# Kernel optimization log

Hardware: AMD Instinct MI355X
Metric: run time of the kernel (lower is better)

Reference implementation:

```python
import jax, jax.numpy as jnp
import numpy as np

N, FEAT, NCLS = 8192, 1024, 64


def setup_inputs() -> dict:
    key = jax.random.key(0)
    k1, k2, k3, k4, k5, k6 = jax.random.split(key, 6)
    x = jax.random.normal(k1, (N, FEAT), dtype=jnp.float32)
    adj = jax.random.uniform(k2, (N, N), dtype=jnp.float32)  # pairwise distances
    stdv1 = 1.0 / np.sqrt(FEAT)
    W1 = jax.random.uniform(k3, (FEAT, FEAT), jnp.float32, -stdv1, stdv1)
    b1 = jax.random.uniform(k4, (FEAT,), jnp.float32, -stdv1, stdv1)
    W2 = jax.random.uniform(k5, (FEAT, NCLS), jnp.float32, -stdv1, stdv1)
    b2 = jax.random.uniform(k6, (NCLS,), jnp.float32, -stdv1, stdv1)
    alpha = jnp.full((1,), 0.3, dtype=jnp.float32)
    return {"x": x, "adj": adj, "W1": W1, "b1": b1, "W2": W2, "b2": b2,
            "alpha": alpha, "K": 32}


def reference(x, adj, W1, b1, W2, b2, alpha, K):
    # --- top-K smallest-distance neighbor selection per row ---
    neg_vals, idx = jax.lax.top_k(-adj, K)        # K smallest adj entries per row
    vals = -neg_vals                              # [N, K] distances
    w = jnp.exp(-alpha[0] * vals)                 # 1 / exp(alpha * d)
    w = w / jnp.sum(w, axis=1, keepdims=True)     # row-normalize edge weights

    def spmm(h):
        # sparse A @ h using top-K edge list: out[i] = sum_k w[i,k] * h[idx[i,k]]
        return jnp.einsum('nk,nkf->nf', w, h[idx])

    # 2-layer GCN path of SimTSC (eval mode: dropout is identity)
    h = jax.nn.relu(spmm(x @ W1) + b1)            # [N, FEAT]
    out = spmm(h @ W2) + b2                       # [N, NCLS]
    return jax.nn.log_softmax(out, axis=1)
```

## Files before the change

### kernel.cpp

```cpp
#include <hip/hip_runtime.h>

typedef __bf16 bf16_t;
typedef __bf16 bf16x4 __attribute__((ext_vector_type(4)));
typedef __bf16 bf16x8 __attribute__((ext_vector_type(8)));
typedef float  f32x4  __attribute__((ext_vector_type(4)));

typedef const __attribute__((address_space(1))) void gvoid_t;
typedef __attribute__((address_space(3))) void lvoid_t;

#define N_NODES 8192
#define FEAT    1024
#define NCLS    64
#define TK      32

__device__ __forceinline__ float wave_min_f32(float v) {
  int x = __float_as_int(v), t;
#define STEPF(ctrl) t = __builtin_amdgcn_update_dpp(x, x, ctrl, 0xf, 0xf, false); \
                    v = fminf(v, __int_as_float(t)); x = __float_as_int(v);
  STEPF(0x111)
  STEPF(0x112)
  STEPF(0x114)
  STEPF(0x118)
  STEPF(0x142)
  STEPF(0x143)
#undef STEPF
  return __int_as_float(__builtin_amdgcn_readlane(x, 63));
}

__device__ __forceinline__ unsigned wave_min_u32(unsigned v) {
  int x = (int)v, t;
#define STEPU(ctrl) t = __builtin_amdgcn_update_dpp(x, x, ctrl, 0xf, 0xf, false); \
                    x = (int)((unsigned)x < (unsigned)t ? (unsigned)x : (unsigned)t);
  STEPU(0x111)
  STEPU(0x112)
  STEPU(0x114)
  STEPU(0x118)
  STEPU(0x142)
  STEPU(0x143)
#undef STEPU
  return (unsigned)__builtin_amdgcn_readlane(x, 63);
}

__global__ __launch_bounds__(256) void topk_kernel(const float* __restrict__ adj,
                                                   const float* __restrict__ alphap,
                                                   const float* __restrict__ x,
                                                   bf16_t* __restrict__ x_bf,
                                                   int* __restrict__ idx_out,
                                                   float* __restrict__ w_out,
                                                   const float* __restrict__ W1,
                                                   bf16_t* __restrict__ W1t,
                                                   const float* __restrict__ W2,
                                                   bf16_t* __restrict__ W2t) {
  const int tid = threadIdx.x;
  __shared__ float tile[64][65];
  __shared__ float svals[256];
  __shared__ int   sidx[256];
  __shared__ int   scnt;

  if (blockIdx.x >= N_NODES) {
    const int tb = blockIdx.x - N_NODES;
    const int bxi = tb % 17, by = tb / 17;
    const float* in;
    bf16_t* out;
    int cols, bx;
    if (bxi < 16) { in = W1; out = W1t; cols = FEAT; bx = bxi; }
    else          { in = W2; out = W2t; cols = NCLS; bx = 0; }
#pragma unroll
    for (int i = 0; i < 16; ++i) {
      int li = i * 256 + tid;
      int r = li >> 6, c = li & 63;
      tile[r][c] = in[(size_t)(by * 64 + r) * cols + bx * 64 + c];
    }
    __syncthreads();
#pragma unroll
    for (int i = 0; i < 16; ++i) {
      int li = i * 256 + tid;
      int r = li >> 6, c = li & 63;
      out[(size_t)(bx * 64 + r) * FEAT + by * 64 + c] = (__bf16)tile[c][r];
    }
    return;
  }

  const int row = blockIdx.x;
  {
    const float4 v = ((const float4*)(x + (size_t)row * FEAT))[tid];
    bf16x4 o;
    o[0] = (__bf16)v.x; o[1] = (__bf16)v.y; o[2] = (__bf16)v.z; o[3] = (__bf16)v.w;
    ((bf16x4*)(x_bf + (size_t)row * FEAT))[tid] = o;
  }

  const float* arow = adj + (size_t)row * N_NODES;
  float thr = 1.0f / 128.0f;
  int cnt = 0;
  for (int attempt = 0; attempt < 24; ++attempt) {
    __syncthreads();
    if (tid == 0) scnt = 0;
    __syncthreads();
#pragma unroll
    for (int v = 0; v < 8; ++v) {
      int vi = v * 256 + tid;
      float4 q = ((const float4*)arow)[vi];
      int base = vi * 4;
      if (q.x < thr) { int p = atomicAdd(&scnt, 1); if (p < 256) { svals[p] = q.x; sidx[p] = base;     } }
      if (q.y < thr) { int p = atomicAdd(&scnt, 1); if (p < 256) { svals[p] = q.y; sidx[p] = base + 1; } }
      if (q.z < thr) { int p = atomicAdd(&scnt, 1); if (p < 256) { svals[p] = q.z; sidx[p] = base + 2; } }
      if (q.w < thr) { int p = atomicAdd(&scnt, 1); if (p < 256) { svals[p] = q.w; sidx[p] = base + 3; } }
    }
    __syncthreads();
    cnt = scnt;
    if (cnt >= TK && cnt <= 256) break;
    thr = (cnt < TK) ? thr * 2.0f : thr * 0.5f;
  }
  const int M = cnt < 256 ? cnt : 256;

  if (tid < 64) {
    const int lane = tid;
    const float INF = __int_as_float(0x7f800000);
    float cv[4];
    int   ci[4];
#pragma unroll
    for (int j = 0; j < 4; ++j) {
      int slot = lane + j * 64;
      if (slot < M) { cv[j] = svals[slot]; ci[j] = sidx[slot]; }
      else          { cv[j] = INF;         ci[j] = 0x7fffffff; }
    }
    float selv = 0.f;
    int   seli = 0;
    for (int k = 0; k < TK; ++k) {
      const float lv = fminf(fminf(cv[0], cv[1]), fminf(cv[2], cv[3]));
      const float wv = wave_min_f32(lv);
      unsigned li = 0xffffffffu;
#pragma unroll
      for (int j = 0; j < 4; ++j)
        if (cv[j] == wv) li = li < (unsigned)ci[j] ? li : (unsigned)ci[j];
      const unsigned wi = wave_min_u32(li);
      if (lane == k) { selv = wv; seli = (int)wi; }
#pragma unroll
      for (int j = 0; j < 4; ++j)
        if (cv[j] == wv && (unsigned)ci[j] == wi) cv[j] = INF;
    }
    const float a = alphap[0];
    const float e = (lane < TK) ? expf(-a * selv) : 0.0f;
    float ssum = e;
#pragma unroll
    for (int off = 1; off < 64; off <<= 1) ssum += __shfl_xor(ssum, off);
    if (lane < TK) {
      idx_out[(size_t)row * TK + lane] = seli & (N_NODES - 1);
      w_out[(size_t)row * TK + lane]   = e / ssum;
    }
  }
}

__global__ __launch_bounds__(256, 2) void gemm1_kernel(const bf16_t* __restrict__ A,
                                                       const bf16_t* __restrict__ Bt,
                                                       bf16_t* __restrict__ C) {
  constexpr int BM = 128, BN = 128, Kd = FEAT;
  constexpr int LDSA = BM * 64;
  constexpr int LDSB = BN * 64;
  __shared__ char lds[2][LDSA + LDSB];
  const int tid = threadIdx.x;
  const int wid = tid >> 6, lane = tid & 63;
  const int b = blockIdx.x;
  const int xcd = b & 7, j = b >> 3;
  const int bm0 = (xcd * 8 + (j >> 3)) * BM;
  const int bn0 = (j & 7) * BN;
  const int wr = wid >> 1, wc = wid & 1;
  constexpr int WM = BM / 2, WN = BN / 2;
  constexpr int NMI = WM / 16, NNI = WN / 16;

  auto stage = [&](int buf, int t) {
    const int k0 = t * 32;
#pragma unroll
    for (int li = 0; li < BM / 64; ++li) {
      const int rb = wid * (BM / 4) + li * 16;
      const int r = rb + (lane >> 2);
      const int sdat = (lane & 3) ^ (r & 3);
      const bf16_t* g = A + (size_t)(bm0 + r) * Kd + k0 + sdat * 8;
      __builtin_amdgcn_global_load_lds((gvoid_t*)g, (lvoid_t*)&lds[buf][rb * 64], 16, 0, 0);
    }
#pragma unroll
    for (int li = 0; li < BN / 64; ++li) {
      const int rb = wid * (BN / 4) + li * 16;
      const int r = rb + (lane >> 2);
      const int sdat = (lane & 3) ^ (r & 3);
      const bf16_t* g = Bt + (size_t)(bn0 + r) * Kd + k0 + sdat * 8;
      __builtin_amdgcn_global_load_lds((gvoid_t*)g, (lvoid_t*)&lds[buf][LDSA + rb * 64], 16, 0, 0);
    }
  };

  f32x4 acc[NMI][NNI];
#pragma unroll
  for (int mi = 0; mi < NMI; ++mi)
#pragma unroll
    for (int ni = 0; ni < NNI; ++ni) acc[mi][ni] = (f32x4){0.f, 0.f, 0.f, 0.f};

  const int nT = Kd / 32;
  stage(0, 0);
  __syncthreads();
  for (int t = 0; t < nT; ++t) {
    const int cur = t & 1;
    if (t + 1 < nT) stage(cur ^ 1, t + 1);
    const char* la = &lds[cur][0];
    const char* lb = &lds[cur][LDSA];
    const int s = lane >> 4;
    bf16x8 af[NMI], bfr[NNI];
#pragma unroll
    for (int mi = 0; mi < NMI; ++mi) {
      const int m = wr * WM + mi * 16 + (lane & 15);
      af[mi] = *(const bf16x8*)(la + m * 64 + ((s ^ (m & 3)) * 16));
    }
#pragma unroll
    for (int ni = 0; ni < NNI; ++ni) {
      const int n = wc * WN + ni * 16 + (lane & 15);
      bfr[ni] = *(const bf16x8*)(lb + n * 64 + ((s ^ (n & 3)) * 16));
    }
#pragma unroll
    for (int mi = 0; mi < NMI; ++mi)
#pragma unroll
      for (int ni = 0; ni < NNI; ++ni)
        acc[mi][ni] = __builtin_amdgcn_mfma_f32_16x16x32_bf16(af[mi], bfr[ni], acc[mi][ni], 0, 0, 0);
    __syncthreads();
  }

#pragma unroll
  for (int mi = 0; mi < NMI; ++mi)
#pragma unroll
    for (int ni = 0; ni < NNI; ++ni)
#pragma unroll
      for (int j4 = 0; j4 < 4; ++j4) {
        const int r = bm0 + wr * WM + mi * 16 + (lane >> 4) * 4 + j4;
        const int c = bn0 + wc * WN + ni * 16 + (lane & 15);
        C[(size_t)r * FEAT + c] = (__bf16)acc[mi][ni][j4];
      }
}

#define SROWS  16
#define SCHUNK 128
#define NCHUNK 8
__global__ __launch_bounds__(256) void spmm_gemm2_kernel(const bf16_t* __restrict__ xW1,
                                                         const int* __restrict__ idxm,
                                                         const float* __restrict__ wm,
                                                         const float* __restrict__ b1,
                                                         const bf16_t* __restrict__ W2t,
                                                         bf16_t* __restrict__ part) {
  const int tid = threadIdx.x;
  const int c  = blockIdx.x & (NCHUNK - 1);
  const int rg = blockIdx.x >> 3;
  const int r0 = rg * SROWS;
  const int f0 = c * SCHUNK;
  __shared__ int    snb[SROWS][TK];
  __shared__ float  swt[SROWS][TK];
  __shared__ bf16_t hls[SROWS][SCHUNK];
  ((int2*)&snb[0][0])[tid]   = ((const int2*)(idxm + (size_t)r0 * TK))[tid];
  ((float2*)&swt[0][0])[tid] = ((const float2*)(wm + (size_t)r0 * TK))[tid];
  __syncthreads();
  const int wid = tid >> 6, lane = tid & 63;
  const int gr = tid >> 4;
  const int gc = (tid & 15) * 8;

  float a[8];
#pragma unroll
  for (int j = 0; j < 8; ++j) a[j] = 0.f;
#pragma unroll 8
  for (int k = 0; k < TK; ++k) {
    const bf16x8 v = *(const bf16x8*)(xW1 + (size_t)snb[gr][k] * FEAT + f0 + gc);
    const float wk = swt[gr][k];
#pragma unroll
    for (int j = 0; j < 8; ++j) a[j] += wk * (float)v[j];
  }
  const float4 b0 = ((const float4*)(b1 + f0 + gc))[0];
  const float4 b1v = ((const float4*)(b1 + f0 + gc))[1];
  bf16x8 o0;
  o0[0] = (__bf16)fmaxf(a[0] + b0.x, 0.f);
  o0[1] = (__bf16)fmaxf(a[1] + b0.y, 0.f);
  o0[2] = (__bf16)fmaxf(a[2] + b0.z, 0.f);
  o0[3] = (__bf16)fmaxf(a[3] + b0.w, 0.f);
  o0[4] = (__bf16)fmaxf(a[4] + b1v.x, 0.f);
  o0[5] = (__bf16)fmaxf(a[5] + b1v.y, 0.f);
  o0[6] = (__bf16)fmaxf(a[6] + b1v.z, 0.f);
  o0[7] = (__bf16)fmaxf(a[7] + b1v.w, 0.f);
  const int g0 = (gc >> 3);
  char* hb = (char*)&hls[0][0];
  *(bf16x8*)(hb + gr * (SCHUNK * 2) + ((g0 ^ (gr & 7)) * 16)) = o0;

  const int s = lane >> 4;
  const int m = lane & 15;
  const int n = wid * 16 + (lane & 15);
  bf16x8 bfr[SCHUNK / 32];
#pragma unroll
  for (int ks = 0; ks < SCHUNK / 32; ++ks)
    bfr[ks] = *(const bf16x8*)(W2t + (size_t)n * FEAT + f0 + ks * 32 + s * 8);
  __syncthreads();

  f32x4 acc = (f32x4){0.f, 0.f, 0.f, 0.f};
  const char* hr = (char*)&hls[0][0] + m * (SCHUNK * 2);
#pragma unroll
  for (int ks = 0; ks < SCHUNK / 32; ++ks) {
    const int g = ks * 4 + s;
    const bf16x8 afrag = *(const bf16x8*)(hr + ((g ^ (m & 7)) * 16));
    acc = __builtin_amdgcn_mfma_f32_16x16x32_bf16(afrag, bfr[ks], acc, 0, 0, 0);
  }
#pragma unroll
  for (int j = 0; j < 4; ++j) {
    const int r = r0 + (lane >> 4) * 4 + j;
    const int col = wid * 16 + (lane & 15);
    part[((size_t)c * N_NODES + r) * NCLS + col] = (__bf16)acc[j];
  }
}

__global__ __launch_bounds__(256) void reduce8_kernel(const bf16_t* __restrict__ part,
                                                      float* __restrict__ out2) {
  const int i = blockIdx.x * 256 + threadIdx.x;
  float s[8];
  {
    const bf16x8 p = ((const bf16x8*)part)[i];
#pragma unroll
    for (int j = 0; j < 8; ++j) s[j] = (float)p[j];
  }
#pragma unroll
  for (int c = 1; c < NCHUNK; ++c) {
    const bf16x8 p = ((const bf16x8*)(part + (size_t)c * N_NODES * NCLS))[i];
#pragma unroll
    for (int j = 0; j < 8; ++j) s[j] += (float)p[j];
  }
  float4 lo, hi;
  lo.x = s[0]; lo.y = s[1]; lo.z = s[2]; lo.w = s[3];
  hi.x = s[4]; hi.y = s[5]; hi.z = s[6]; hi.w = s[7];
  ((float4*)out2)[i * 2]     = lo;
  ((float4*)out2)[i * 2 + 1] = hi;
}

__global__ __launch_bounds__(256) void final_kernel(const float* __restrict__ out2,
                                                    const int* __restrict__ idxm,
                                                    const float* __restrict__ wm,
                                                    const float* __restrict__ b2,
                                                    float* __restrict__ out) {
  const int wid = threadIdx.x >> 6, lane = threadIdx.x & 63;
  const int row = blockIdx.x * 4 + wid;
  const int kk = lane & 31;
  const float wv = wm[(size_t)row * TK + kk];
  const int   iv = idxm[(size_t)row * TK + kk];
  float acc = 0.f;
#pragma unroll 8
  for (int k = 0; k < TK; ++k) {
    const float wk = __shfl(wv, k);
    const int   ik = __shfl(iv, k);
    acc += wk * out2[(size_t)ik * NCLS + lane];
  }
  const float logit = acc + b2[lane];
  float m = logit;
#pragma unroll
  for (int off = 1; off < 64; off <<= 1) m = fmaxf(m, __shfl_xor(m, off));
  const float e = expf(logit - m);
  float ssum = e;
#pragma unroll
  for (int off = 1; off < 64; off <<= 1) ssum += __shfl_xor(ssum, off);
  out[(size_t)row * NCLS + lane] = (logit - m) - logf(ssum);
}

extern "C" void kernel_launch(void* const* d_in, const int* in_sizes, int n_in,
                              void* d_out, int out_size, void* d_ws, size_t ws_size,
                              hipStream_t stream) {
  (void)in_sizes; (void)n_in; (void)out_size; (void)ws_size;
  const float* x     = (const float*)d_in[0];
  const float* adj   = (const float*)d_in[1];
  const float* W1    = (const float*)d_in[2];
  const float* b1    = (const float*)d_in[3];
  const float* W2    = (const float*)d_in[4];
  const float* b2    = (const float*)d_in[5];
  const float* alpha = (const float*)d_in[6];

  char* ws = (char*)d_ws;
  const size_t MB = 1024 * 1024;
  bf16_t* x_bf = (bf16_t*)(ws + 0 * MB);
  bf16_t* xW1  = (bf16_t*)(ws + 16 * MB);
  bf16_t* W1t  = (bf16_t*)(ws + 48 * MB);
  bf16_t* W2t  = (bf16_t*)(ws + 50 * MB);
  float*  out2 = (float*)(ws + 51 * MB);
  int*    idxm = (int*)(ws + 53 * MB);
  float*  wm   = (float*)(ws + 54 * MB);
  bf16_t* part = (bf16_t*)(ws + 56 * MB);

  topk_kernel<<<dim3(N_NODES + 272), dim3(256), 0, stream>>>(
      adj, alpha, x, x_bf, idxm, wm, W1, W1t, W2, W2t);
  gemm1_kernel<<<dim3(512), dim3(256), 0, stream>>>(x_bf, W1t, xW1);
  spmm_gemm2_kernel<<<dim3((N_NODES / SROWS) * NCHUNK), dim3(256), 0, stream>>>(
      xW1, idxm, wm, b1, W2t, part);
  reduce8_kernel<<<dim3(N_NODES * NCLS / 8 / 256), dim3(256), 0, stream>>>(part, out2);
  final_kernel<<<dim3(N_NODES / 4), dim3(256), 0, stream>>>(out2, idxm, wm, b2, (float*)d_out);
}
```

Before: 135.0 us.

## Fuse top-K selection with the first GEMM into one interleaved kernel

The x conversion and weight transposes move into a small prep kernel. Top-K row selection and the x@W1 GEMM tiles are merged into one launch, with one GEMM block interleaved among every 16 top-K blocks. The bandwidth-bound adjacency scan can then overlap with MFMA-bound GEMM work, and one launch boundary goes away. In exchange, top-K blocks now reserve the GEMM's large LDS allocation and run at the GEMM's occupancy bound, which may cut how many scan blocks fit per CU.

```diff
diff --git a/kernel.cpp b/kernel.cpp
--- a/kernel.cpp
+++ b/kernel.cpp
@@ -41,73 +41,164 @@
   return (unsigned)__builtin_amdgcn_readlane(x, 63);
 }
 
-__global__ __launch_bounds__(256) void topk_kernel(const float* __restrict__ adj,
-                                                   const float* __restrict__ alphap,
-                                                   const float* __restrict__ x,
-                                                   bf16_t* __restrict__ x_bf,
-                                                   int* __restrict__ idx_out,
-                                                   float* __restrict__ w_out,
-                                                   const float* __restrict__ W1,
+__global__ __launch_bounds__(256) void prep_kernel(const float* __restrict__ W1,
                                                    bf16_t* __restrict__ W1t,
                                                    const float* __restrict__ W2,
-                                                   bf16_t* __restrict__ W2t) {
+                                                   bf16_t* __restrict__ W2t,
+                                                   const float* __restrict__ x,
+                                                   bf16_t* __restrict__ x_bf) {
   const int tid = threadIdx.x;
+  const int b = blockIdx.x;
+  if (b < 2048) {
+#pragma unroll
+    for (int i = 0; i < 4; ++i) {
+      const int idx = b * 1024 + i * 256 + tid;
+      const float4 v = ((const float4*)x)[idx];
+      bf16x4 o;
+      o[0] = (__bf16)v.x; o[1] = (__bf16)v.y; o[2] = (__bf16)v.z; o[3] = (__bf16)v.w;
+      ((bf16x4*)x_bf)[idx] = o;
+    }
+    return;
+  }
   __shared__ float tile[64][65];
-  __shared__ float svals[256];
-  __shared__ int   sidx[256];
-  __shared__ int   scnt;
-
-  if (blockIdx.x >= N_NODES) {
-    const int tb = blockIdx.x - N_NODES;
-    const int bxi = tb % 17, by = tb / 17;
-    const float* in;
-    bf16_t* out;
-    int cols, bx;
-    if (bxi < 16) { in = W1; out = W1t; cols = FEAT; bx = bxi; }
-    else          { in = W2; out = W2t; cols = NCLS; bx = 0; }
-#pragma unroll
-    for (int i = 0; i < 16; ++i) {
-      int li = i * 256 + tid;
-      int r = li >> 6, c = li & 63;
-      tile[r][c] = in[(size_t)(by * 64 + r) * cols + bx * 64 + c];
-    }
+  const int tb = b - 2048;
+  const int bxi = tb % 17, by = tb / 17;
+  const float* in;
+  bf16_t* out;
+  int cols, bx;
+  if (bxi < 16) { in = W1; out = W1t; cols = FEAT; bx = bxi; }
+  else          { in = W2; out = W2t; cols = NCLS; bx = 0; }
+#pragma unroll
+  for (int i = 0; i < 16; ++i) {
+    int li = i * 256 + tid;
+    int r = li >> 6, c = li & 63;
+    tile[r][c] = in[(size_t)(by * 64 + r) * cols + bx * 64 + c];
+  }
+  __syncthreads();
+#pragma unroll
+  for (int i = 0; i < 16; ++i) {
+    int li = i * 256 + tid;
+    int r = li >> 6, c = li & 63;
+    out[(size_t)(bx * 64 + r) * FEAT + by * 64 + c] = (__bf16)tile[c][r];
+  }
+}
+
+#define FUSED_BLOCKS (512 * 17)
+__global__ __launch_bounds__(256, 2) void fused_kernel(const float* __restrict__ adj,
+                                                       const float* __restrict__ alphap,
+                                                       const bf16_t* __restrict__ x_bf,
+                                                       const bf16_t* __restrict__ W1t,
+                                                       bf16_t* __restrict__ xW1,
+                                                       int* __restrict__ idx_out,
+                                                       float* __restrict__ w_out) {
+  constexpr int BM = 128, BN = 128, Kd = FEAT;
+  constexpr int LDSA = BM * 64;
+  constexpr int LDSB = BN * 64;
+  __shared__ char smem[2 * (LDSA + LDSB)];
+  const int tid = threadIdx.x;
+  const int b = blockIdx.x;
+  const int j = b / 17;
+
+  if (b % 17 == 0) {
+    auto lds = (char(*)[LDSA + LDSB])smem;
+    const int wid = tid >> 6, lane = tid & 63;
+    const int xcd = j & 7, jj = j >> 3;
+    const int bm0 = (xcd * 8 + (jj >> 3)) * BM;
+    const int bn0 = (jj & 7) * BN;
+    const int wr = wid >> 1, wc = wid & 1;
+    constexpr int WM = BM / 2, WN = BN / 2;
+    constexpr int NMI = WM / 16, NNI = WN / 16;
+
+    auto stage = [&](int buf, int t) {
+      const int k0 = t * 32;
+#pragma unroll
+      for (int li = 0; li < BM / 64; ++li) {
+        const int rb = wid * (BM / 4) + li * 16;
+        const int r = rb + (lane >> 2);
+        const int sdat = (lane & 3) ^ (r & 3);
+        const bf16_t* g = x_bf + (size_t)(bm0 + r) * Kd + k0 + sdat * 8;
+        __builtin_amdgcn_global_load_lds((gvoid_t*)g, (lvoid_t*)&lds[buf][rb * 64], 16, 0, 0);
+      }
+#pragma unroll
+      for (int li = 0; li < BN / 64; ++li) {
+        const int rb = wid * (BN / 4) + li * 16;
+        const int r = rb + (lane >> 2);
+        const int sdat = (lane & 3) ^ (r & 3);
+        const bf16_t* g = W1t + (size_t)(bn0 + r) * Kd + k0 + sdat * 8;
+        __builtin_amdgcn_global_load_lds((gvoid_t*)g, (lvoid_t*)&lds[buf][LDSA + rb * 64], 16, 0, 0);
+      }
+    };
+
+    f32x4 acc[NMI][NNI];
+#pragma unroll
+    for (int mi = 0; mi < NMI; ++mi)
+#pragma unroll
+      for (int ni = 0; ni < NNI; ++ni) acc[mi][ni] = (f32x4){0.f, 0.f, 0.f, 0.f};
+
+    const int nT = Kd / 32;
+    stage(0, 0);
     __syncthreads();
-#pragma unroll
-    for (int i = 0; i < 16; ++i) {
-      int li = i * 256 + tid;
-      int r = li >> 6, c = li & 63;
-      out[(size_t)(bx * 64 + r) * FEAT + by * 64 + c] = (__bf16)tile[c][r];
-    }
+    for (int t = 0; t < nT; ++t) {
+      const int cur = t & 1;
+      if (t + 1 < nT) stage(cur ^ 1, t + 1);
+      const char* la = &lds[cur][0];
+      const char* lb = &lds[cur][LDSA];
+      const int s = lane >> 4;
+      bf16x8 af[NMI], bfr[NNI];
+#pragma unroll
+      for (int mi = 0; mi < NMI; ++mi) {
+        const int m = wr * WM + mi * 16 + (lane & 15);
+        af[mi] = *(const bf16x8*)(la + m * 64 + ((s ^ (m & 3)) * 16));
+      }
+#pragma unroll
+      for (int ni = 0; ni < NNI; ++ni) {
+        const int n = wc * WN + ni * 16 + (lane & 15);
+        bfr[ni] = *(const bf16x8*)(lb + n * 64 + ((s ^ (n & 3)) * 16));
+      }
+#pragma unroll
+      for (int mi = 0; mi < NMI; ++mi)
+#pragma unroll
+        for (int ni = 0; ni < NNI; ++ni)
+          acc[mi][ni] = __builtin_amdgcn_mfma_f32_16x16x32_bf16(af[mi], bfr[ni], acc[mi][ni], 0, 0, 0);
+      __syncthreads();
+    }
+
+#pragma unroll
+    for (int mi = 0; mi < NMI; ++mi)
+#pragma unroll
+      for (int ni = 0; ni < NNI; ++ni)
+#pragma unroll
+        for (int j4 = 0; j4 < 4; ++j4) {
+          const int r = bm0 + wr * WM + mi * 16 + (lane >> 4) * 4 + j4;
+          const int c = bn0 + wc * WN + ni * 16 + (lane & 15);
+          xW1[(size_t)r * FEAT + c] = (__bf16)acc[mi][ni][j4];
+        }
     return;
   }
 
-  const int row = blockIdx.x;
-  {
-    const float4 v = ((const float4*)(x + (size_t)row * FEAT))[tid];
-    bf16x4 o;
-    o[0] = (__bf16)v.x; o[1] = (__bf16)v.y; o[2] = (__bf16)v.z; o[3] = (__bf16)v.w;
-    ((bf16x4*)(x_bf + (size_t)row * FEAT))[tid] = o;
-  }
-
+  float* svals = (float*)smem;
+  int*   sidx  = (int*)(smem + 1024);
+  int*   scnt  = (int*)(smem + 2048);
+  const int row = b - j - 1;
   const float* arow = adj + (size_t)row * N_NODES;
   float thr = 1.0f / 128.0f;
   int cnt = 0;
   for (int attempt = 0; attempt < 24; ++attempt) {
     __syncthreads();
-    if (tid == 0) scnt = 0;
+    if (tid == 0) *scnt = 0;
     __syncthreads();
 #pragma unroll
     for (int v = 0; v < 8; ++v) {
       int vi = v * 256 + tid;
       float4 q = ((const float4*)arow)[vi];
       int base = vi * 4;
-      if (q.x < thr) { int p = atomicAdd(&scnt, 1); if (p < 256) { svals[p] = q.x; sidx[p] = base;     } }
-      if (q.y < thr) { int p = atomicAdd(&scnt, 1); if (p < 256) { svals[p] = q.y; sidx[p] = base + 1; } }
-      if (q.z < thr) { int p = atomicAdd(&scnt, 1); if (p < 256) { svals[p] = q.z; sidx[p] = base + 2; } }
-      if (q.w < thr) { int p = atomicAdd(&scnt, 1); if (p < 256) { svals[p] = q.w; sidx[p] = base + 3; } }
+      if (q.x < thr) { int p = atomicAdd(scnt, 1); if (p < 256) { svals[p] = q.x; sidx[p] = base;     } }
+      if (q.y < thr) { int p = atomicAdd(scnt, 1); if (p < 256) { svals[p] = q.y; sidx[p] = base + 1; } }
+      if (q.z < thr) { int p = atomicAdd(scnt, 1); if (p < 256) { svals[p] = q.z; sidx[p] = base + 2; } }
+      if (q.w < thr) { int p = atomicAdd(scnt, 1); if (p < 256) { svals[p] = q.w; sidx[p] = base + 3; } }
     }
     __syncthreads();
-    cnt = scnt;
+    cnt = *scnt;
     if (cnt >= TK && cnt <= 256) break;
     thr = (cnt < TK) ? thr * 2.0f : thr * 0.5f;
   }
@@ -119,10 +210,10 @@
     float cv[4];
     int   ci[4];
 #pragma unroll
-    for (int j = 0; j < 4; ++j) {
-      int slot = lane + j * 64;
-      if (slot < M) { cv[j] = svals[slot]; ci[j] = sidx[slot]; }
-      else          { cv[j] = INF;         ci[j] = 0x7fffffff; }
+    for (int jq = 0; jq < 4; ++jq) {
+      int slot = lane + jq * 64;
+      if (slot < M) { cv[jq] = svals[slot]; ci[jq] = sidx[slot]; }
+      else          { cv[jq] = INF;         ci[jq] = 0x7fffffff; }
     }
     float selv = 0.f;
     int   seli = 0;
@@ -131,13 +222,13 @@
       const float wv = wave_min_f32(lv);
       unsigned li = 0xffffffffu;
 #pragma unroll
-      for (int j = 0; j < 4; ++j)
-        if (cv[j] == wv) li = li < (unsigned)ci[j] ? li : (unsigned)ci[j];
+      for (int jq = 0; jq < 4; ++jq)
+        if (cv[jq] == wv) li = li < (unsigned)ci[jq] ? li : (unsigned)ci[jq];
       const unsigned wi = wave_min_u32(li);
       if (lane == k) { selv = wv; seli = (int)wi; }
 #pragma unroll
-      for (int j = 0; j < 4; ++j)
-        if (cv[j] == wv && (unsigned)ci[j] == wi) cv[j] = INF;
+      for (int jq = 0; jq < 4; ++jq)
+        if (cv[jq] == wv && (unsigned)ci[jq] == wi) cv[jq] = INF;
     }
     const float a = alphap[0];
     const float e = (lane < TK) ? expf(-a * selv) : 0.0f;
@@ -149,89 +240,6 @@
       w_out[(size_t)row * TK + lane]   = e / ssum;
     }
   }
-}
-
-__global__ __launch_bounds__(256, 2) void gemm1_kernel(const bf16_t* __restrict__ A,
-                                                       const bf16_t* __restrict__ Bt,
-                                                       bf16_t* __restrict__ C) {
-  constexpr int BM = 128, BN = 128, Kd = FEAT;
-  constexpr int LDSA = BM * 64;
-  constexpr int LDSB = BN * 64;
-  __shared__ char lds[2][LDSA + LDSB];
-  const int tid = threadIdx.x;
-  const int wid = tid >> 6, lane = tid & 63;
-  const int b = blockIdx.x;
-  const int xcd = b & 7, j = b >> 3;
-  const int bm0 = (xcd * 8 + (j >> 3)) * BM;
-  const int bn0 = (j & 7) * BN;
-  const int wr = wid >> 1, wc = wid & 1;
-  constexpr int WM = BM / 2, WN = BN / 2;
-  constexpr int NMI = WM / 16, NNI = WN / 16;
-
-  auto stage = [&](int buf, int t) {
-    const int k0 = t * 32;
-#pragma unroll
-    for (int li = 0; li < BM / 64; ++li) {
-      const int rb = wid * (BM / 4) + li * 16;
-      const int r = rb + (lane >> 2);
-      const int sdat = (lane & 3) ^ (r & 3);
-      const bf16_t* g = A + (size_t)(bm0 + r) * Kd + k0 + sdat * 8;
-      __builtin_amdgcn_global_load_lds((gvoid_t*)g, (lvoid_t*)&lds[buf][rb * 64], 16, 0, 0);
-    }
-#pragma unroll
-    for (int li = 0; li < BN / 64; ++li) {
-      const int rb = wid * (BN / 4) + li * 16;
-      const int r = rb + (lane >> 2);
-      const int sdat = (lane & 3) ^ (r & 3);
-      const bf16_t* g = Bt + (size_t)(bn0 + r) * Kd + k0 + sdat * 8;
-      __builtin_amdgcn_global_load_lds((gvoid_t*)g, (lvoid_t*)&lds[buf][LDSA + rb * 64], 16, 0, 0);
-    }
-  };
-
-  f32x4 acc[NMI][NNI];
-#pragma unroll
-  for (int mi = 0; mi < NMI; ++mi)
-#pragma unroll
-    for (int ni = 0; ni < NNI; ++ni) acc[mi][ni] = (f32x4){0.f, 0.f, 0.f, 0.f};
-
-  const int nT = Kd / 32;
-  stage(0, 0);
-  __syncthreads();
-  for (int t = 0; t < nT; ++t) {
-    const int cur = t & 1;
-    if (t + 1 < nT) stage(cur ^ 1, t + 1);
-    const char* la = &lds[cur][0];
-    const char* lb = &lds[cur][LDSA];
-    const int s = lane >> 4;
-    bf16x8 af[NMI], bfr[NNI];
-#pragma unroll
-    for (int mi = 0; mi < NMI; ++mi) {
-      const int m = wr * WM + mi * 16 + (lane & 15);
-      af[mi] = *(const bf16x8*)(la + m * 64 + ((s ^ (m & 3)) * 16));
-    }
-#pragma unroll
-    for (int ni = 0; ni < NNI; ++ni) {
-      const int n = wc * WN + ni * 16 + (lane & 15);
-      bfr[ni] = *(const bf16x8*)(lb + n * 64 + ((s ^ (n & 3)) * 16));
-    }
-#pragma unroll
-    for (int mi = 0; mi < NMI; ++mi)
-#pragma unroll
-      for (int ni = 0; ni < NNI; ++ni)
-        acc[mi][ni] = __builtin_amdgcn_mfma_f32_16x16x32_bf16(af[mi], bfr[ni], acc[mi][ni], 0, 0, 0);
-    __syncthreads();
-  }
-
-#pragma unroll
-  for (int mi = 0; mi < NMI; ++mi)
-#pragma unroll
-    for (int ni = 0; ni < NNI; ++ni)
-#pragma unroll
-      for (int j4 = 0; j4 < 4; ++j4) {
-        const int r = bm0 + wr * WM + mi * 16 + (lane >> 4) * 4 + j4;
-        const int c = bn0 + wc * WN + ni * 16 + (lane & 15);
-        C[(size_t)r * FEAT + c] = (__bf16)acc[mi][ni][j4];
-      }
 }
 
 #define SROWS  16
@@ -381,9 +389,9 @@
   float*  wm   = (float*)(ws + 54 * MB);
   bf16_t* part = (bf16_t*)(ws + 56 * MB);
 
-  topk_kernel<<<dim3(N_NODES + 272), dim3(256), 0, stream>>>(
-      adj, alpha, x, x_bf, idxm, wm, W1, W1t, W2, W2t);
-  gemm1_kernel<<<dim3(512), dim3(256), 0, stream>>>(x_bf, W1t, xW1);
+  prep_kernel<<<dim3(2048 + 272), dim3(256), 0, stream>>>(W1, W1t, W2, W2t, x, x_bf);
+  fused_kernel<<<dim3(FUSED_BLOCKS), dim3(256), 0, stream>>>(
+      adj, alpha, x_bf, W1t, xW1, idxm, wm);
   spmm_gemm2_kernel<<<dim3((N_NODES / SROWS) * NCHUNK), dim3(256), 0, stream>>>(
       xW1, idxm, wm, b1, W2t, part);
   reduce8_kernel<<<dim3(N_NODES * NCLS / 8 / 256), dim3(256), 0, stream>>>(part, out2);
```

Measured after the change: 168.9 us. 1.25x slower.
